# Optimization experiments

Measured on AMD Instinct MI355X. Metric: run time of the kernel, lower is better.

The kernel has to match this reference:

```python
import jax, jax.numpy as jnp
import numpy as np

N = 50000          # nodes
E = 800000         # edges (before self-loops)
F_IN, F_HID, F_OUT = 128, 64, 64
NEG_SLOPE_ATT = 0.2   # GATConv internal leaky_relu
NEG_SLOPE_ACT = 0.01  # F.leaky_relu default between layers


def setup_inputs() -> dict:
    key = jax.random.key(0)
    ks = jax.random.split(key, 16)

    def glorot(k, shape):
        fan = float(sum(shape)) if len(shape) > 1 else float(shape[0])
        return jax.random.normal(k, shape, jnp.float32) * (2.0 / fan) ** 0.5

    return {
        "x": jax.random.normal(ks[0], (N, F_IN), jnp.float32),
        "edge_index": jax.random.randint(ks[1], (2, E), 0, N, dtype=jnp.int64),
        "W1": glorot(ks[2], (F_IN, F_HID)),
        "a_src1": glorot(ks[3], (F_HID,)),
        "a_dst1": glorot(ks[4], (F_HID,)),
        "b1": jnp.zeros((F_HID,), jnp.float32),
        "W2": glorot(ks[5], (F_HID, F_HID)),
        "a_src2": glorot(ks[6], (F_HID,)),
        "a_dst2": glorot(ks[7], (F_HID,)),
        "b2": jnp.zeros((F_HID,), jnp.float32),
        "W3": glorot(ks[8], (F_HID, F_OUT)),
        "a_src3": glorot(ks[9], (F_OUT,)),
        "a_dst3": glorot(ks[10], (F_OUT,)),
        "b3": jnp.zeros((F_OUT,), jnp.float32),
    }


def gat_conv(h, src, dst, W, a_src, a_dst, b):
    # Single-head PyG GATConv: project, per-edge scores, segment softmax over dst, scatter-add.
    z = h @ W                              # [N, C]
    e_src = z @ a_src                      # [N]
    e_dst = z @ a_dst                      # [N]
    e = jax.nn.leaky_relu(e_src[src] + e_dst[dst], NEG_SLOPE_ATT)  # [E']
    m = jax.ops.segment_max(e, dst, num_segments=N)
    ex = jnp.exp(e - m[dst])
    denom = jax.ops.segment_sum(ex, dst, num_segments=N)
    alpha = ex / (denom[dst] + 1e-16)      # segment softmax (PyG adds 1e-16)
    out = jax.ops.segment_sum(alpha[:, None] * z[src], dst, num_segments=N) + b
    return out, alpha


def reference(x, edge_index, W1, a_src1, a_dst1, b1, W2, a_src2, a_dst2, b2, W3, a_src3, a_dst3, b3):
    # add_self_loops=True (GATConv default): append (i, i) for every node
    loops = jnp.arange(N, dtype=edge_index.dtype)
    ei = jnp.concatenate([edge_index, jnp.stack([loops, loops])], axis=1)  # [2, E+N]
    src, dst = ei[0], ei[1]

    h = x
    alpha = None
    for (W, asr, ads, b) in ((W1, a_src1, a_dst1, b1),
                             (W2, a_src2, a_dst2, b2),
                             (W3, a_src3, a_dst3, b3)):
        h, alpha = gat_conv(h, src, dst, W, asr, ads, b)
        h = jax.nn.leaky_relu(h, NEG_SLOPE_ACT)
    return (h, ei, alpha)
```

## Files before the change

kernel.cpp:

```cpp
#include <hip/hip_runtime.h>
#include <hip/hip_bf16.h>
#include <hip/hip_fp8.h>

#define NN 50000
#define EE 800000
#define E2 850000
#define F_IN 128
#define F_HID 64
#define NCHUNK ((NN + 255) / 256)
#define NTILE  ((NN + 63) / 64)
#define SLICES 512
#define SCHUNK ((E2 + SLICES - 1) / SLICES)
#define AGGB 2048

__device__ __forceinline__ unsigned char f32_to_fp8(float x) {
    __hip_fp8_e4m3 t(x);
    return t.__x;
}
__device__ __forceinline__ float fp8_to_f32(unsigned char b) {
    __hip_fp8_e4m3 t; t.__x = b;
    return (float)t;
}
__device__ __forceinline__ float readlane_f(float v, int l) {
    return __uint_as_float(__builtin_amdgcn_readlane(__float_as_uint(v), l));
}

__global__ __launch_bounds__(256) void hist_ei_kernel(const int* __restrict__ ei,
                                                      int* __restrict__ deg,
                                                      float* __restrict__ ei_out) {
    int e = blockIdx.x * 256 + threadIdx.x;
    if (e >= E2) return;
    int s, d;
    if (e < EE) { s = ei[e]; d = ei[EE + e]; }
    else        { s = d = e - EE; }
    atomicAdd(&deg[d], 1);
    ei_out[e]      = (float)s;
    ei_out[E2 + e] = (float)d;
}

__global__ __launch_bounds__(256) void scan_part12(const int* __restrict__ deg,
                                                   int* __restrict__ csum,
                                                   int* __restrict__ ticket) {
    int i = blockIdx.x * 256 + threadIdx.x;
    int v = (i < NN) ? deg[i] : 0;
#pragma unroll
    for (int d = 32; d; d >>= 1) v += __shfl_xor(v, d);
    __shared__ int ws[4];
    if ((threadIdx.x & 63) == 0) ws[threadIdx.x >> 6] = v;
    __syncthreads();
    __shared__ int isLast;
    if (threadIdx.x == 0) {
        atomicExch(&csum[blockIdx.x], ws[0] + ws[1] + ws[2] + ws[3]);
        __threadfence();
        isLast = (atomicAdd(ticket, 1) == gridDim.x - 1) ? 1 : 0;
    }
    __syncthreads();
    if (isLast) {
        __threadfence();
        __shared__ int sd[256];
        int t = threadIdx.x;
        int v2 = (t < NCHUNK) ? atomicAdd(&csum[t], 0) : 0;
        sd[t] = v2;
        __syncthreads();
        for (int off = 1; off < 256; off <<= 1) {
            int o = (t >= off) ? sd[t - off] : 0;
            __syncthreads();
            sd[t] += o;
            __syncthreads();
        }
        if (t < NCHUNK) atomicExch(&csum[t], sd[t] - v2);
    }
}

__global__ __launch_bounds__(256) void scan_part3(const int* __restrict__ deg,
                                                  const int* __restrict__ csum,
                                                  int* __restrict__ offs,
                                                  int* __restrict__ cursor) {
    __shared__ int sd[256];
    int t = threadIdx.x;
    int i = blockIdx.x * 256 + t;
    int v = (i < NN) ? deg[i] : 0;
    sd[t] = v;
    __syncthreads();
    for (int off = 1; off < 256; off <<= 1) {
        int o = (t >= off) ? sd[t - off] : 0;
        __syncthreads();
        sd[t] += o;
        __syncthreads();
    }
    if (i < NN) {
        int ex = sd[t] - v + csum[blockIdx.x];
        offs[i] = ex;
        cursor[i] = ex;
    }
}

__global__ __launch_bounds__(256) void scatter_kernel(const int* __restrict__ ei,
                                                      int* __restrict__ cursor,
                                                      int* __restrict__ src_sorted) {
    int g = blockIdx.x & 7;
    int slice = blockIdx.x >> 3;
    int begin = slice * SCHUNK;
    int end = begin + SCHUNK; if (end > E2) end = E2;
    for (int e = begin + threadIdx.x; e < end; e += 256) {
        int s, d;
        if (e < EE) { s = ei[e]; d = ei[EE + e]; }
        else        { s = d = e - EE; }
        int bucket = (d * 8) / NN;
        if (bucket == g) {
            int pos = atomicAdd(&cursor[d], 1);
            src_sorted[pos] = s;
        }
    }
}

template <int K>
__global__ __launch_bounds__(256) void gemm_tile(const float* __restrict__ h,
                                                 const float* __restrict__ W,
                                                 const float* __restrict__ a_src,
                                                 const float* __restrict__ a_dst,
                                                 unsigned char* __restrict__ z8,
                                                 float* __restrict__ es,
                                                 float* __restrict__ ed) {
    constexpr int LDA = K + 4;
    __shared__ float Alds[64 * LDA];
    __shared__ float Blds[K * 64];

    int tid = threadIdx.x;
    int base = blockIdx.x * 64;

    {
        constexpr int F4R = K / 4;
        for (int t = tid; t < 64 * F4R; t += 256) {
            int r = t / F4R;
            int c4 = t % F4R;
            int gr = base + r;
            if (gr >= NN) gr = NN - 1;
            float4 v = *(const float4*)(h + (size_t)gr * K + c4 * 4);
            *(float4*)(&Alds[r * LDA + c4 * 4]) = v;
        }
    }
    for (int t = tid; t < K * 16; t += 256) {
        float4 v = *(const float4*)(W + t * 4);
        *(float4*)(&Blds[t * 4]) = v;
    }
    __syncthreads();

    int tx = tid & 15;
    int ty = tid >> 4;

    float acc[4][4] = {};
#pragma unroll 4
    for (int k = 0; k < K; k += 4) {
        float4 a[4], b[4];
#pragma unroll
        for (int i = 0; i < 4; ++i)
            a[i] = *(const float4*)(&Alds[(4 * ty + i) * LDA + k]);
#pragma unroll
        for (int kk = 0; kk < 4; ++kk)
            b[kk] = *(const float4*)(&Blds[(k + kk) * 64 + 4 * tx]);
#pragma unroll
        for (int i = 0; i < 4; ++i) {
            acc[i][0] = fmaf(a[i].x, b[0].x, acc[i][0]);
            acc[i][1] = fmaf(a[i].x, b[0].y, acc[i][1]);
            acc[i][2] = fmaf(a[i].x, b[0].z, acc[i][2]);
            acc[i][3] = fmaf(a[i].x, b[0].w, acc[i][3]);
            acc[i][0] = fmaf(a[i].y, b[1].x, acc[i][0]);
            acc[i][1] = fmaf(a[i].y, b[1].y, acc[i][1]);
            acc[i][2] = fmaf(a[i].y, b[1].z, acc[i][2]);
            acc[i][3] = fmaf(a[i].y, b[1].w, acc[i][3]);
            acc[i][0] = fmaf(a[i].z, b[2].x, acc[i][0]);
            acc[i][1] = fmaf(a[i].z, b[2].y, acc[i][1]);
            acc[i][2] = fmaf(a[i].z, b[2].z, acc[i][2]);
            acc[i][3] = fmaf(a[i].z, b[2].w, acc[i][3]);
            acc[i][0] = fmaf(a[i].w, b[3].x, acc[i][0]);
            acc[i][1] = fmaf(a[i].w, b[3].y, acc[i][1]);
            acc[i][2] = fmaf(a[i].w, b[3].z, acc[i][2]);
            acc[i][3] = fmaf(a[i].w, b[3].w, acc[i][3]);
        }
    }

    float4 as4 = *(const float4*)(a_src + 4 * tx);
    float4 ad4 = *(const float4*)(a_dst + 4 * tx);
    float ps[4], pd[4];
#pragma unroll
    for (int i = 0; i < 4; ++i) {
        int gr = base + 4 * ty + i;
        if (gr < NN) {
            unsigned int pk = (unsigned int)f32_to_fp8(acc[i][0])
                            | ((unsigned int)f32_to_fp8(acc[i][1]) << 8)
                            | ((unsigned int)f32_to_fp8(acc[i][2]) << 16)
                            | ((unsigned int)f32_to_fp8(acc[i][3]) << 24);
            *(unsigned int*)(&z8[(size_t)gr * 64 + 4 * tx]) = pk;
        }
        ps[i] = acc[i][0] * as4.x + acc[i][1] * as4.y + acc[i][2] * as4.z + acc[i][3] * as4.w;
        pd[i] = acc[i][0] * ad4.x + acc[i][1] * ad4.y + acc[i][2] * ad4.z + acc[i][3] * ad4.w;
    }
#pragma unroll
    for (int d = 1; d < 16; d <<= 1) {
#pragma unroll
        for (int i = 0; i < 4; ++i) {
            ps[i] += __shfl_xor(ps[i], d);
            pd[i] += __shfl_xor(pd[i], d);
        }
    }
    if (tx == 0) {
#pragma unroll
        for (int i = 0; i < 4; ++i) {
            int gr = base + 4 * ty + i;
            if (gr < NN) { es[gr] = ps[i]; ed[gr] = pd[i]; }
        }
    }
}

__global__ __launch_bounds__(256) void aggregate(const int* __restrict__ offs,
                                                 const int* __restrict__ deg,
                                                 const int* __restrict__ src_sorted,
                                                 const float* __restrict__ es,
                                                 const float* __restrict__ ed,
                                                 const unsigned char* __restrict__ z8,
                                                 const float* __restrict__ bias,
                                                 float* __restrict__ hout,
                                                 float* __restrict__ denom_out) {
    int tid = threadIdx.x;
    int lane = tid & 63;
    int wave = blockIdx.x * 4 + (tid >> 6);
    const int NW = AGGB * 4;
    float bi = bias[lane];

    int n = wave;
    if (n >= NN) return;
    n = __builtin_amdgcn_readfirstlane(n);
    int off = offs[n];
    int dg = deg[n];
    float edn = ed[n];
    int sv = src_sorted[off + ((lane < dg) ? lane : 0)];

    while (true) {
        int n2 = n + NW;
        bool more = (n2 < NN);
        int off2 = 0, dg2 = 0; float edn2 = 0.f;
        if (more) {
            n2 = __builtin_amdgcn_readfirstlane(n2);
            off2 = offs[n2]; dg2 = deg[n2]; edn2 = ed[n2];
        }

        float dsum = 0.f;
        float a0 = 0.f, a1 = 0.f, a2 = 0.f, a3 = 0.f;
        float a4 = 0.f, a5 = 0.f, a6 = 0.f, a7 = 0.f;
        for (int b0 = 0; b0 < dg; b0 += 64) {
            int bl = dg - b0; if (bl > 64) bl = 64;
            int svb = (b0 == 0) ? sv
                                : src_sorted[off + b0 + ((lane < bl) ? lane : 0)];
            float e = es[svb] + edn;
            e = (e > 0.f) ? e : 0.2f * e;
            float w = (lane < bl) ? __expf(e) : 0.f;
            dsum += w;

            int j = 0;
            for (; j + 8 <= bl; j += 8) {
                int   s0 = __builtin_amdgcn_readlane(svb, j);
                int   s1 = __builtin_amdgcn_readlane(svb, j + 1);
                int   s2 = __builtin_amdgcn_readlane(svb, j + 2);
                int   s3 = __builtin_amdgcn_readlane(svb, j + 3);
                int   s4 = __builtin_amdgcn_readlane(svb, j + 4);
                int   s5 = __builtin_amdgcn_readlane(svb, j + 5);
                int   s6 = __builtin_amdgcn_readlane(svb, j + 6);
                int   s7 = __builtin_amdgcn_readlane(svb, j + 7);
                float w0 = readlane_f(w, j),     w1 = readlane_f(w, j + 1);
                float w2 = readlane_f(w, j + 2), w3 = readlane_f(w, j + 3);
                float w4 = readlane_f(w, j + 4), w5 = readlane_f(w, j + 5);
                float w6 = readlane_f(w, j + 6), w7 = readlane_f(w, j + 7);
                a0 = fmaf(w0, fp8_to_f32(z8[(size_t)s0 * 64 + lane]), a0);
                a1 = fmaf(w1, fp8_to_f32(z8[(size_t)s1 * 64 + lane]), a1);
                a2 = fmaf(w2, fp8_to_f32(z8[(size_t)s2 * 64 + lane]), a2);
                a3 = fmaf(w3, fp8_to_f32(z8[(size_t)s3 * 64 + lane]), a3);
                a4 = fmaf(w4, fp8_to_f32(z8[(size_t)s4 * 64 + lane]), a4);
                a5 = fmaf(w5, fp8_to_f32(z8[(size_t)s5 * 64 + lane]), a5);
                a6 = fmaf(w6, fp8_to_f32(z8[(size_t)s6 * 64 + lane]), a6);
                a7 = fmaf(w7, fp8_to_f32(z8[(size_t)s7 * 64 + lane]), a7);
            }
            for (; j + 4 <= bl; j += 4) {
                int   s0 = __builtin_amdgcn_readlane(svb, j);
                int   s1 = __builtin_amdgcn_readlane(svb, j + 1);
                int   s2 = __builtin_amdgcn_readlane(svb, j + 2);
                int   s3 = __builtin_amdgcn_readlane(svb, j + 3);
                float w0 = readlane_f(w, j),     w1 = readlane_f(w, j + 1);
                float w2 = readlane_f(w, j + 2), w3 = readlane_f(w, j + 3);
                a0 = fmaf(w0, fp8_to_f32(z8[(size_t)s0 * 64 + lane]), a0);
                a1 = fmaf(w1, fp8_to_f32(z8[(size_t)s1 * 64 + lane]), a1);
                a2 = fmaf(w2, fp8_to_f32(z8[(size_t)s2 * 64 + lane]), a2);
                a3 = fmaf(w3, fp8_to_f32(z8[(size_t)s3 * 64 + lane]), a3);
            }
            for (; j < bl; ++j) {
                int   s0 = __builtin_amdgcn_readlane(svb, j);
                float w0 = readlane_f(w, j);
                a0 = fmaf(w0, fp8_to_f32(z8[(size_t)s0 * 64 + lane]), a0);
            }
        }

        int sv2 = 0;
        if (more) sv2 = src_sorted[off2 + ((lane < dg2) ? lane : 0)];

#pragma unroll
        for (int d = 32; d; d >>= 1) dsum += __shfl_xor(dsum, d);
        float acc = ((a0 + a1) + (a2 + a3)) + ((a4 + a5) + (a6 + a7));
        float inv = 1.f / (dsum + 1e-16f);
        float o = acc * inv + bi;
        o = (o > 0.f) ? o : 0.01f * o;
        hout[(size_t)n * 64 + lane] = o;
        if (lane == 0) denom_out[n] = dsum;

        if (!more) break;
        n = n2; off = off2; dg = dg2; edn = edn2; sv = sv2;
    }
}

__global__ __launch_bounds__(256) void alpha_kernel(const int* __restrict__ ei,
                                                    const float* __restrict__ es,
                                                    const float* __restrict__ ed,
                                                    const float* __restrict__ denom,
                                                    float* __restrict__ alpha_out) {
    int e = blockIdx.x * 256 + threadIdx.x;
    if (e >= E2) return;
    int s, d;
    if (e < EE) { s = ei[e]; d = ei[EE + e]; }
    else        { s = d = e - EE; }
    float x = es[s] + ed[d];
    x = (x > 0.f) ? x : 0.2f * x;
    alpha_out[e] = __expf(x) / (denom[d] + 1e-16f);
}

extern "C" void kernel_launch(void* const* d_in, const int* in_sizes, int n_in,
                              void* d_out, int out_size, void* d_ws, size_t ws_size,
                              hipStream_t stream) {
    const float* x   = (const float*)d_in[0];
    const int*   ei  = (const int*)d_in[1];
    const float* W1  = (const float*)d_in[2];
    const float* as1 = (const float*)d_in[3];
    const float* ad1 = (const float*)d_in[4];
    const float* b1  = (const float*)d_in[5];
    const float* W2  = (const float*)d_in[6];
    const float* as2 = (const float*)d_in[7];
    const float* ad2 = (const float*)d_in[8];
    const float* b2  = (const float*)d_in[9];
    const float* W3  = (const float*)d_in[10];
    const float* as3 = (const float*)d_in[11];
    const float* ad3 = (const float*)d_in[12];
    const float* b3  = (const float*)d_in[13];

    float* out       = (float*)d_out;
    float* h_out     = out;
    float* ei_out    = out + (size_t)NN * 64;
    float* alpha_out = ei_out + 2 * (size_t)E2;

    char* w = (char*)d_ws;
    auto carve = [&](size_t bytes) {
        void* p = (void*)w;
        w += (bytes + 255) & ~size_t(255);
        return p;
    };
    float* h1  = (float*)carve((size_t)NN * 64 * 4);
    float* h2  = (float*)carve((size_t)NN * 64 * 4);
    unsigned char* z8 = (unsigned char*)carve((size_t)NN * 64);
    float* es  = (float*)carve((size_t)NN * 4);
    float* ed  = (float*)carve((size_t)NN * 4);
    float* denom = (float*)carve((size_t)NN * 4);
    int* deg        = (int*)carve(((size_t)NN + 64) * 4);
    int* ticket     = deg + NN;
    int* offs       = (int*)carve((size_t)NN * 4);
    int* cursor     = (int*)carve((size_t)NN * 4);
    int* csum       = (int*)carve((size_t)NCHUNK * 4);
    int* src_sorted = (int*)carve((size_t)E2 * 4);

    const int EB = (E2 + 255) / 256;

    hipMemsetAsync(deg, 0, ((size_t)NN + 64) * 4, stream);
    hist_ei_kernel<<<EB, 256, 0, stream>>>(ei, deg, ei_out);
    scan_part12<<<NCHUNK, 256, 0, stream>>>(deg, csum, ticket);
    scan_part3<<<NCHUNK, 256, 0, stream>>>(deg, csum, offs, cursor);
    scatter_kernel<<<SLICES * 8, 256, 0, stream>>>(ei, cursor, src_sorted);

    gemm_tile<F_IN><<<NTILE, 256, 0, stream>>>(x, W1, as1, ad1, z8, es, ed);
    aggregate<<<AGGB, 256, 0, stream>>>(offs, deg, src_sorted, es, ed, z8, b1, h1, denom);
    gemm_tile<F_HID><<<NTILE, 256, 0, stream>>>(h1, W2, as2, ad2, z8, es, ed);
    aggregate<<<AGGB, 256, 0, stream>>>(offs, deg, src_sorted, es, ed, z8, b2, h2, denom);
    gemm_tile<F_HID><<<NTILE, 256, 0, stream>>>(h2, W3, as3, ad3, z8, es, ed);
    aggregate<<<AGGB, 256, 0, stream>>>(offs, deg, src_sorted, es, ed, z8, b3, h_out, denom);
    alpha_kernel<<<EB, 256, 0, stream>>>(ei, es, ed, denom, alpha_out);
}
```

Measured before the change: 315.1 us.

## Aggregate four edges per wave with 4-byte fp8 gathers; simplify scatter

Measured after the change: 313.4 us. About the same (-0.5%).

```diff
diff --git a/kernel.cpp b/kernel.cpp
--- a/kernel.cpp
+++ b/kernel.cpp
@@ -9,8 +9,6 @@
 #define F_HID 64
 #define NCHUNK ((NN + 255) / 256)
 #define NTILE  ((NN + 63) / 64)
-#define SLICES 512
-#define SCHUNK ((E2 + SLICES - 1) / SLICES)
 #define AGGB 2048
 
 __device__ __forceinline__ unsigned char f32_to_fp8(float x) {
@@ -20,9 +18,6 @@
 __device__ __forceinline__ float fp8_to_f32(unsigned char b) {
     __hip_fp8_e4m3 t; t.__x = b;
     return (float)t;
-}
-__device__ __forceinline__ float readlane_f(float v, int l) {
-    return __uint_as_float(__builtin_amdgcn_readlane(__float_as_uint(v), l));
 }
 
 __global__ __launch_bounds__(256) void hist_ei_kernel(const int* __restrict__ ei,
@@ -98,20 +93,13 @@
 __global__ __launch_bounds__(256) void scatter_kernel(const int* __restrict__ ei,
                                                       int* __restrict__ cursor,
                                                       int* __restrict__ src_sorted) {
-    int g = blockIdx.x & 7;
-    int slice = blockIdx.x >> 3;
-    int begin = slice * SCHUNK;
-    int end = begin + SCHUNK; if (end > E2) end = E2;
-    for (int e = begin + threadIdx.x; e < end; e += 256) {
-        int s, d;
-        if (e < EE) { s = ei[e]; d = ei[EE + e]; }
-        else        { s = d = e - EE; }
-        int bucket = (d * 8) / NN;
-        if (bucket == g) {
-            int pos = atomicAdd(&cursor[d], 1);
-            src_sorted[pos] = s;
-        }
-    }
+    int e = blockIdx.x * 256 + threadIdx.x;
+    if (e >= E2) return;
+    int s, d;
+    if (e < EE) { s = ei[e]; d = ei[EE + e]; }
+    else        { s = d = e - EE; }
+    int pos = atomicAdd(&cursor[d], 1);
+    src_sorted[pos] = s;
 }
 
 template <int K>
@@ -226,7 +214,11 @@
     int lane = tid & 63;
     int wave = blockIdx.x * 4 + (tid >> 6);
     const int NW = AGGB * 4;
-    float bi = bias[lane];
+
+    int sub  = lane >> 4;
+    int fgrp = (lane & 15) * 4;
+    const unsigned char* zp = z8 + fgrp;
+    float4 bi4 = *(const float4*)(bias + fgrp);
 
     int n = wave;
     if (n >= NN) return;
@@ -247,7 +239,6 @@
 
         float dsum = 0.f;
         float a0 = 0.f, a1 = 0.f, a2 = 0.f, a3 = 0.f;
-        float a4 = 0.f, a5 = 0.f, a6 = 0.f, a7 = 0.f;
         for (int b0 = 0; b0 < dg; b0 += 64) {
             int bl = dg - b0; if (bl > 64) bl = 64;
             int svb = (b0 == 0) ? sv
@@ -257,58 +248,73 @@
             float w = (lane < bl) ? __expf(e) : 0.f;
             dsum += w;
 
+            int ng = (bl + 3) >> 2;
             int j = 0;
-            for (; j + 8 <= bl; j += 8) {
-                int   s0 = __builtin_amdgcn_readlane(svb, j);
-                int   s1 = __builtin_amdgcn_readlane(svb, j + 1);
-                int   s2 = __builtin_amdgcn_readlane(svb, j + 2);
-                int   s3 = __builtin_amdgcn_readlane(svb, j + 3);
-                int   s4 = __builtin_amdgcn_readlane(svb, j + 4);
-                int   s5 = __builtin_amdgcn_readlane(svb, j + 5);
-                int   s6 = __builtin_amdgcn_readlane(svb, j + 6);
-                int   s7 = __builtin_amdgcn_readlane(svb, j + 7);
-                float w0 = readlane_f(w, j),     w1 = readlane_f(w, j + 1);
-                float w2 = readlane_f(w, j + 2), w3 = readlane_f(w, j + 3);
-                float w4 = readlane_f(w, j + 4), w5 = readlane_f(w, j + 5);
-                float w6 = readlane_f(w, j + 6), w7 = readlane_f(w, j + 7);
-                a0 = fmaf(w0, fp8_to_f32(z8[(size_t)s0 * 64 + lane]), a0);
-                a1 = fmaf(w1, fp8_to_f32(z8[(size_t)s1 * 64 + lane]), a1);
-                a2 = fmaf(w2, fp8_to_f32(z8[(size_t)s2 * 64 + lane]), a2);
-                a3 = fmaf(w3, fp8_to_f32(z8[(size_t)s3 * 64 + lane]), a3);
-                a4 = fmaf(w4, fp8_to_f32(z8[(size_t)s4 * 64 + lane]), a4);
-                a5 = fmaf(w5, fp8_to_f32(z8[(size_t)s5 * 64 + lane]), a5);
-                a6 = fmaf(w6, fp8_to_f32(z8[(size_t)s6 * 64 + lane]), a6);
-                a7 = fmaf(w7, fp8_to_f32(z8[(size_t)s7 * 64 + lane]), a7);
+            for (; j + 4 <= ng; j += 4) {
+                int i0 = 4 * j + sub;
+                int   s0 = __shfl(svb, i0);
+                int   s1 = __shfl(svb, i0 + 4);
+                int   s2 = __shfl(svb, i0 + 8);
+                int   s3 = __shfl(svb, i0 + 12);
+                float w0 = __shfl(w, i0);
+                float w1 = __shfl(w, i0 + 4);
+                float w2 = __shfl(w, i0 + 8);
+                float w3 = __shfl(w, i0 + 12);
+                unsigned int v0 = *(const unsigned int*)(zp + (size_t)s0 * 64);
+                unsigned int v1 = *(const unsigned int*)(zp + (size_t)s1 * 64);
+                unsigned int v2 = *(const unsigned int*)(zp + (size_t)s2 * 64);
+                unsigned int v3 = *(const unsigned int*)(zp + (size_t)s3 * 64);
+                a0 = fmaf(w0, fp8_to_f32(v0 & 255), a0);
+                a1 = fmaf(w0, fp8_to_f32((v0 >> 8) & 255), a1);
+                a2 = fmaf(w0, fp8_to_f32((v0 >> 16) & 255), a2);
+                a3 = fmaf(w0, fp8_to_f32(v0 >> 24), a3);
+                a0 = fmaf(w1, fp8_to_f32(v1 & 255), a0);
+                a1 = fmaf(w1, fp8_to_f32((v1 >> 8) & 255), a1);
+                a2 = fmaf(w1, fp8_to_f32((v1 >> 16) & 255), a2);
+                a3 = fmaf(w1, fp8_to_f32(v1 >> 24), a3);
+                a0 = fmaf(w2, fp8_to_f32(v2 & 255), a0);
+                a1 = fmaf(w2, fp8_to_f32((v2 >> 8) & 255), a1);
+                a2 = fmaf(w2, fp8_to_f32((v2 >> 16) & 255), a2);
+                a3 = fmaf(w2, fp8_to_f32(v2 >> 24), a3);
+                a0 = fmaf(w3, fp8_to_f32(v3 & 255), a0);
+                a1 = fmaf(w3, fp8_to_f32((v3 >> 8) & 255), a1);
+                a2 = fmaf(w3, fp8_to_f32((v3 >> 16) & 255), a2);
+                a3 = fmaf(w3, fp8_to_f32(v3 >> 24), a3);
             }
-            for (; j + 4 <= bl; j += 4) {
-                int   s0 = __builtin_amdgcn_readlane(svb, j);
-                int   s1 = __builtin_amdgcn_readlane(svb, j + 1);
-                int   s2 = __builtin_amdgcn_readlane(svb, j + 2);
-                int   s3 = __builtin_amdgcn_readlane(svb, j + 3);
-                float w0 = readlane_f(w, j),     w1 = readlane_f(w, j + 1);
-                float w2 = readlane_f(w, j + 2), w3 = readlane_f(w, j + 3);
-                a0 = fmaf(w0, fp8_to_f32(z8[(size_t)s0 * 64 + lane]), a0);
-                a1 = fmaf(w1, fp8_to_f32(z8[(size_t)s1 * 64 + lane]), a1);
-                a2 = fmaf(w2, fp8_to_f32(z8[(size_t)s2 * 64 + lane]), a2);
-                a3 = fmaf(w3, fp8_to_f32(z8[(size_t)s3 * 64 + lane]), a3);
-            }
-            for (; j < bl; ++j) {
-                int   s0 = __builtin_amdgcn_readlane(svb, j);
-                float w0 = readlane_f(w, j);
-                a0 = fmaf(w0, fp8_to_f32(z8[(size_t)s0 * 64 + lane]), a0);
+            for (; j < ng; ++j) {
+                int i0 = 4 * j + sub;
+                int   s0 = __shfl(svb, i0);
+                float w0 = __shfl(w, i0);
+                unsigned int v0 = *(const unsigned int*)(zp + (size_t)s0 * 64);
+                a0 = fmaf(w0, fp8_to_f32(v0 & 255), a0);
+                a1 = fmaf(w0, fp8_to_f32((v0 >> 8) & 255), a1);
+                a2 = fmaf(w0, fp8_to_f32((v0 >> 16) & 255), a2);
+                a3 = fmaf(w0, fp8_to_f32(v0 >> 24), a3);
             }
         }
 
         int sv2 = 0;
         if (more) sv2 = src_sorted[off2 + ((lane < dg2) ? lane : 0)];
 
+        a0 += __shfl_xor(a0, 16); a1 += __shfl_xor(a1, 16);
+        a2 += __shfl_xor(a2, 16); a3 += __shfl_xor(a3, 16);
+        a0 += __shfl_xor(a0, 32); a1 += __shfl_xor(a1, 32);
+        a2 += __shfl_xor(a2, 32); a3 += __shfl_xor(a3, 32);
 #pragma unroll
         for (int d = 32; d; d >>= 1) dsum += __shfl_xor(dsum, d);
-        float acc = ((a0 + a1) + (a2 + a3)) + ((a4 + a5) + (a6 + a7));
         float inv = 1.f / (dsum + 1e-16f);
-        float o = acc * inv + bi;
-        o = (o > 0.f) ? o : 0.01f * o;
-        hout[(size_t)n * 64 + lane] = o;
+        if (lane < 16) {
+            float4 o;
+            o.x = a0 * inv + bi4.x;
+            o.y = a1 * inv + bi4.y;
+            o.z = a2 * inv + bi4.z;
+            o.w = a3 * inv + bi4.w;
+            o.x = (o.x > 0.f) ? o.x : 0.01f * o.x;
+            o.y = (o.y > 0.f) ? o.y : 0.01f * o.y;
+            o.z = (o.z > 0.f) ? o.z : 0.01f * o.z;
+            o.w = (o.w > 0.f) ? o.w : 0.01f * o.w;
+            *(float4*)(hout + (size_t)n * 64 + fgrp) = o;
+        }
         if (lane == 0) denom_out[n] = dsum;
 
         if (!more) break;
@@ -379,7 +385,7 @@
     hist_ei_kernel<<<EB, 256, 0, stream>>>(ei, deg, ei_out);
     scan_part12<<<NCHUNK, 256, 0, stream>>>(deg, csum, ticket);
     scan_part3<<<NCHUNK, 256, 0, stream>>>(deg, csum, offs, cursor);
-    scatter_kernel<<<SLICES * 8, 256, 0, stream>>>(ei, cursor, src_sorted);
+    scatter_kernel<<<EB, 256, 0, stream>>>(ei, cursor, src_sorted);
 
     gemm_tile<F_IN><<<NTILE, 256, 0, stream>>>(x, W1, as1, ad1, z8, es, ed);
     aggregate<<<AGGB, 256, 0, stream>>>(offs, deg, src_sorted, es, ed, z8, b1, h1, denom);
```
